# Kernel tuning notes

Measured on AMD Instinct MI355X. Metric: run time of the kernel, lower is better.

Reference implementation:

```python
import jax, jax.numpy as jnp
import numpy as np

DIM = 256
HEAD_DIM = 32
HEADS = DIM // HEAD_DIM
SHAPE = (64, 64)          # (H, W) patch grid
WS = 8                    # window size
SHIFT = 4                 # shift size (ws // 2)
SCALE = HEAD_DIM ** -0.5
WS2 = WS * WS


def _rel_indices(ws):
    # relative position index for every (query, key) pair in a window
    a = np.arange(ws)
    y1, x1, y2, x2 = np.meshgrid(a, a, a, a, indexing='ij')
    idx = (y1 - y2 + ws - 1) * (2 * ws - 1) + (x1 - x2 + ws - 1)
    return idx.reshape(ws * ws, ws * ws)  # (ws2, ws2)


def _shift_mask(shape, ws, shift):
    # region labels per patch, 9 regions from the 3x3 slice grid
    H, W = shape
    region = np.zeros((H, W), dtype=np.int32)
    slices = [slice(0, -ws), slice(-ws, -shift), slice(-shift, None)]
    num = 0
    for i in slices:
        for j in slices:
            region[i, j] = num
            num += 1
    # window-partition the region map -> (n_windows, ws2)
    nH, nW = H // ws, W // ws
    r = region.reshape(nH, ws, nW, ws).transpose(0, 2, 1, 3).reshape(nH * nW, ws * ws)
    # True where query and key come from different regions
    return (r[:, None, :] - r[:, :, None]) != 0  # (nw, ws2, ws2)


REL_IDX = jnp.asarray(_rel_indices(WS))                 # (ws2, ws2) int
MASK = jnp.asarray(_shift_mask(SHAPE, WS, SHIFT))       # (nw, ws2, ws2) bool


def _split_windows(x, ws):
    # (b, H, W, C) -> (b * nH * nW, ws*ws, C)
    b, H, W, C = x.shape
    x = x.reshape(b, H // ws, ws, W // ws, ws, C)
    x = x.transpose(0, 1, 3, 2, 4, 5)
    return x.reshape(-1, ws * ws, C)


def _merge_windows(x, shape, ws):
    # inverse of _split_windows
    H, W = shape
    nH, nW = H // ws, W // ws
    C = x.shape[-1]
    x = x.reshape(-1, nH, nW, ws, ws, C)
    x = x.transpose(0, 1, 3, 2, 4, 5)
    return x.reshape(-1, H, W, C)


def setup_inputs() -> dict:
    key = jax.random.key(0)
    ks = jax.random.split(key, 6)
    s = 0.02
    return {
        'x': jax.random.normal(ks[0], (32, SHAPE[0] * SHAPE[1], DIM), jnp.float32),
        'w_qkv': jax.random.normal(ks[1], (3 * DIM, DIM), jnp.float32) * s,
        'b_qkv': jax.random.normal(ks[2], (3 * DIM,), jnp.float32) * s,
        'w_out': jax.random.normal(ks[3], (DIM, DIM), jnp.float32) * s,
        'b_out': jax.random.normal(ks[4], (DIM,), jnp.float32) * s,
        'pos_enc': jax.random.normal(ks[5], (HEADS, (2 * WS - 1) ** 2), jnp.float32) * s,
    }


def reference(x, w_qkv, b_qkv, w_out, b_out, pos_enc):
    B, N, C = x.shape
    H, W = SHAPE
    nw = (H // WS) * (W // WS)

    xg = x.reshape(B, H, W, C)
    if SHIFT > 0:
        xg = jnp.roll(xg, (-SHIFT, -SHIFT), axis=(1, 2))
    xw = _split_windows(xg, WS)                        # (B*nw, ws2, C)

    qkv = xw @ w_qkv.T + b_qkv                         # (B*nw, ws2, 3C)
    qkv = qkv.reshape(-1, WS2, 3, HEADS, HEAD_DIM)
    q, k, v = (qkv[:, :, i].transpose(0, 2, 1, 3) for i in range(3))  # (Bn, h, ws2, hd)

    attn = jnp.einsum('bhqd,bhkd->bhqk', q, k) * SCALE  # (Bn, h, ws2, ws2)
    bias = pos_enc[:, REL_IDX]                          # (h, ws2, ws2)
    attn = attn + bias[None]

    if SHIFT > 0:
        attn = attn.reshape(B, nw, HEADS, WS2, WS2)
        attn = jnp.where(MASK[None, :, None], -jnp.inf, attn)
        attn = attn.reshape(B * nw, HEADS, WS2, WS2)

    attn = jax.nn.softmax(attn, axis=-1)
    out = jnp.einsum('bhqk,bhkd->bhqd', attn, v)        # (Bn, h, ws2, hd)
    out = out.transpose(0, 2, 1, 3).reshape(-1, WS2, C)
    out = out @ w_out.T + b_out                         # (Bn, ws2, C)

    out = _merge_windows(out, SHAPE, WS)                # (B, H, W, C)
    if SHIFT > 0:
        out = jnp.roll(out, (SHIFT, SHIFT), axis=(1, 2))
    return out.reshape(B, N, C)
```

## Files before the change

kernel.cpp:

```cpp
#include <hip/hip_runtime.h>
#include <stdint.h>


typedef short short8 __attribute__((ext_vector_type(8)));
typedef float f32x4 __attribute__((ext_vector_type(4)));

typedef __attribute__((address_space(1))) uint32_t g_u32;
typedef __attribute__((address_space(3))) uint32_t l_u32;

#define SCALE 0.17677669529663687f

__device__ __forceinline__ uint16_t f2bf(float f) {
  union { float f; uint32_t u; } c; c.f = f;
  uint32_t r = c.u + 0x7FFFu + ((c.u >> 16) & 1u);
  return (uint16_t)(r >> 16);
}

__device__ __forceinline__ void g2lds16(const void* g, void* l) {
  __builtin_amdgcn_global_load_lds((const g_u32*)g, (l_u32*)l, 16, 0, 0);
}

__global__ __launch_bounds__(256) void cvtx_kernel(const float* __restrict__ x,
                                                   uint16_t* __restrict__ xb) {
  int tid = threadIdx.x;
  int token = blockIdx.x * 8 + (tid >> 5);
  int c = (tid & 31) * 8;
  int w = token >> 6, t = token & 63;
  int b = w >> 6, wd = w & 63;
  int h = (wd >> 3) * 8 + (t >> 3);
  int xx = (wd & 7) * 8 + (t & 7);
  int src = b * 4096 + (((h + 4) & 63) << 6) + ((xx + 4) & 63);
  const float* sp = x + (size_t)src * 256 + c;
  f32x4 a = *(const f32x4*)sp;
  f32x4 d = *(const f32x4*)(sp + 4);
  short8 v;
  v[0] = (short)f2bf(a[0]); v[1] = (short)f2bf(a[1]);
  v[2] = (short)f2bf(a[2]); v[3] = (short)f2bf(a[3]);
  v[4] = (short)f2bf(d[0]); v[5] = (short)f2bf(d[1]);
  v[6] = (short)f2bf(d[2]); v[7] = (short)f2bf(d[3]);
  *(short8*)&xb[(size_t)token * 256 + c] = v;
}

__global__ __launch_bounds__(256) void cvt_kernel(const float* __restrict__ in,
                                                  uint16_t* __restrict__ out, int n) {
  int i = (blockIdx.x * 256 + threadIdx.x) * 8;
  if (i >= n) return;
  f32x4 a = *(const f32x4*)(in + i);
  f32x4 b = *(const f32x4*)(in + i + 4);
  short8 v;
  v[0] = (short)f2bf(a[0]); v[1] = (short)f2bf(a[1]);
  v[2] = (short)f2bf(a[2]); v[3] = (short)f2bf(a[3]);
  v[4] = (short)f2bf(b[0]); v[5] = (short)f2bf(b[1]);
  v[6] = (short)f2bf(b[2]); v[7] = (short)f2bf(b[3]);
  *(short8*)(out + i) = v;
}

__global__ __launch_bounds__(256) void bias_kernel(const float* __restrict__ pe,
                                                   float* __restrict__ bm) {
  int bx = blockIdx.x;
  int wd = bx >> 3, head = bx & 7;
  int hw = wd >> 3, ww = wd & 7;
  int tid = threadIdx.x;
  int kk = tid >> 2, a0 = (tid & 3) * 4;
  int jy = kk >> 3, jx = kk & 7;
  int hj = hw * 8 + jy, xj = ww * 8 + jx;
  int rj = (hj >= 60 ? 2 : (hj >= 56 ? 1 : 0)) * 3 + (xj >= 60 ? 2 : (xj >= 56 ? 1 : 0));
  float* dst = bm + (size_t)bx * 4096 + kk * 64 + a0 * 4;
  for (int aa = 0; aa < 4; ++aa) {
    int a = a0 + aa;
    f32x4 v;
#pragma unroll
    for (int ni = 0; ni < 4; ++ni) {
      int i = ni * 16 + a;
      int iy = i >> 3, ix = i & 7;
      int hi = hw * 8 + iy, xi = ww * 8 + ix;
      int ri = (hi >= 60 ? 2 : (hi >= 56 ? 1 : 0)) * 3 + (xi >= 60 ? 2 : (xi >= 56 ? 1 : 0));
      v[ni] = (ri != rj) ? -1e30f : pe[head * 225 + (iy - jy + 7) * 15 + (ix - jx + 7)];
    }
    *(f32x4*)(dst + aa * 4) = v;
  }
}

__global__ __launch_bounds__(256) void qkv_kernel(
    const uint16_t* __restrict__ xb, const uint16_t* __restrict__ wq,
    const float* __restrict__ bqkv,
    uint16_t* __restrict__ qws, uint16_t* __restrict__ kws, uint16_t* __restrict__ vws) {
  __shared__ uint16_t sm[16384];
  uint16_t* As = sm;
  uint16_t* Bs = sm + 4096;
  const int tid = threadIdx.x, lane = tid & 63, wv = tid >> 6;
  const int quad = lane >> 4, l15 = lane & 15;
  const int n0 = blockIdx.x * 128;
  const int m0 = blockIdx.y * 128;

  const int c0 = wv * 2, c1 = c0 + 1;
  const uint16_t* ap0 = xb + (size_t)(m0 + c0 * 16 + (lane >> 2)) * 256 + (lane & 3) * 8;
  const uint16_t* ap1 = xb + (size_t)(m0 + c1 * 16 + (lane >> 2)) * 256 + (lane & 3) * 8;
  const uint16_t* bp0 = wq + (size_t)(n0 + c0 * 16 + (lane >> 2)) * 256 + (lane & 3) * 8;
  const uint16_t* bp1 = wq + (size_t)(n0 + c1 * 16 + (lane >> 2)) * 256 + (lane & 3) * 8;

  const int wm = (wv & 1) * 64, wn = (wv >> 1) * 64;
  f32x4 zero = {0.f, 0.f, 0.f, 0.f};
  f32x4 acc[4][4];
#pragma unroll
  for (int mi = 0; mi < 4; ++mi)
#pragma unroll
    for (int ni = 0; ni < 4; ++ni) acc[mi][ni] = zero;

  for (int ks = 0; ks < 8; ++ks) {
    int k0 = ks * 32;
    g2lds16(ap0 + k0, &As[c0 * 512]);
    g2lds16(ap1 + k0, &As[c1 * 512]);
    g2lds16(bp0 + k0, &Bs[c0 * 512]);
    g2lds16(bp1 + k0, &Bs[c1 * 512]);
    __syncthreads();
    short8 af[4], bf[4];
#pragma unroll
    for (int mi = 0; mi < 4; ++mi)
      af[mi] = *(const short8*)&As[(wm + mi * 16 + l15) * 32 + quad * 8];
#pragma unroll
    for (int ni = 0; ni < 4; ++ni)
      bf[ni] = *(const short8*)&Bs[(wn + ni * 16 + l15) * 32 + quad * 8];
#pragma unroll
    for (int mi = 0; mi < 4; ++mi)
#pragma unroll
      for (int ni = 0; ni < 4; ++ni)
        acc[mi][ni] = __builtin_amdgcn_mfma_f32_16x16x32_bf16(af[mi], bf[ni], acc[mi][ni], 0, 0, 0);
    __syncthreads();
  }

  float bq4[4];
#pragma unroll
  for (int ni = 0; ni < 4; ++ni) bq4[ni] = bqkv[n0 + wn + ni * 16 + l15];
  const int ng0 = n0 + wn;
  const int sct = ng0 >> 8;
  uint16_t* epi = sm + wv * 4096;

  if (sct < 2) {
#pragma unroll
    for (int mi = 0; mi < 4; ++mi)
#pragma unroll
      for (int ni = 0; ni < 4; ++ni)
#pragma unroll
        for (int r = 0; r < 4; ++r) {
          int t = mi * 16 + quad * 4 + r, n = ni * 16 + l15;
          epi[t * 64 + ((((n >> 3) ^ (t & 7)) << 3) | (n & 7))] = f2bf(acc[mi][ni][r] + bq4[ni]);
        }
    uint16_t* dst = (sct == 0) ? qws : kws;
    const int tb = m0 + wm;
#pragma unroll
    for (int cc = 0; cc < 8; ++cc) {
      int chunk = cc * 64 + lane;
      int trow = chunk >> 3, part = chunk & 7;
      short8 v = *(const short8*)&epi[trow * 64 + ((part ^ (trow & 7)) << 3)];
      int tok = tb + trow, w = tok >> 6, t = tok & 63;
      int ng = ng0 + part * 8, hd = (ng >> 5) & 7, d = ng & 31;
      *(short8*)&dst[(size_t)((w * 8 + hd) * 64 + t) * 32 + d] = v;
    }
  } else {
#pragma unroll
    for (int mi = 0; mi < 4; ++mi)
#pragma unroll
      for (int ni = 0; ni < 4; ++ni)
#pragma unroll
        for (int r = 0; r < 4; ++r) {
          int t = mi * 16 + quad * 4 + r, n = ni * 16 + l15;
          epi[n * 64 + ((((t >> 3) ^ (n & 7)) << 3) | (t & 7))] = f2bf(acc[mi][ni][r] + bq4[ni]);
        }
    const int tb = m0 + wm;
#pragma unroll
    for (int cc = 0; cc < 8; ++cc) {
      int chunk = cc * 64 + lane;
      int drow = chunk >> 3, part = chunk & 7;
      short8 v = *(const short8*)&epi[drow * 64 + ((part ^ (drow & 7)) << 3)];
      int ng = ng0 + drow, hd = (ng >> 5) & 7, d = ng & 31;
      int tok = tb + part * 8, w = tok >> 6, t = tok & 63;
      *(short8*)&vws[(size_t)((w * 8 + hd) * 32 + d) * 64 + t] = v;
    }
  }
}

__global__ __launch_bounds__(256) void attn_kernel(
    const uint16_t* __restrict__ qws, const uint16_t* __restrict__ kws,
    const uint16_t* __restrict__ vws, const float* __restrict__ bm,
    uint16_t* __restrict__ ao) {
  __shared__ uint16_t P[4][4096];
  const int tid = threadIdx.x, lane = tid & 63, wv = tid >> 6;
  const int quad = lane >> 4, l15 = lane & 15;
  const int gid = blockIdx.x * 4 + wv;
  const int w = gid >> 3, head = gid & 7;
  const uint16_t* qb = qws + (size_t)(w * 8 + head) * 2048;
  const uint16_t* kb = kws + (size_t)(w * 8 + head) * 2048;
  const uint16_t* vb = vws + (size_t)(w * 8 + head) * 2048;
  const float* bmh = bm + (size_t)((w & 63) * 8 + head) * 4096;
  f32x4 zero = {0.f, 0.f, 0.f, 0.f};

  short8 ak[4], bq[4];
#pragma unroll
  for (int mi = 0; mi < 4; ++mi)
    ak[mi] = *(const short8*)&kb[(mi * 16 + l15) * 32 + quad * 8];
#pragma unroll
  for (int ni = 0; ni < 4; ++ni)
    bq[ni] = *(const short8*)&qb[(ni * 16 + l15) * 32 + quad * 8];

  f32x4 s[4][4];
#pragma unroll
  for (int mi = 0; mi < 4; ++mi)
#pragma unroll
    for (int ni = 0; ni < 4; ++ni)
      s[mi][ni] = __builtin_amdgcn_mfma_f32_16x16x32_bf16(ak[mi], bq[ni], zero, 0, 0, 0);

#pragma unroll
  for (int mi = 0; mi < 4; ++mi)
#pragma unroll
    for (int r = 0; r < 4; ++r) {
      int kk = mi * 16 + quad * 4 + r;
      f32x4 b4 = *(const f32x4*)&bmh[kk * 64 + l15 * 4];
#pragma unroll
      for (int ni = 0; ni < 4; ++ni)
        s[mi][ni][r] = s[mi][ni][r] * SCALE + b4[ni];
    }

#pragma unroll
  for (int ni = 0; ni < 4; ++ni) {
    float mx = s[0][ni][0];
#pragma unroll
    for (int mi = 0; mi < 4; ++mi)
#pragma unroll
      for (int r = 0; r < 4; ++r) mx = fmaxf(mx, s[mi][ni][r]);
    mx = fmaxf(mx, __shfl_xor(mx, 16, 64));
    mx = fmaxf(mx, __shfl_xor(mx, 32, 64));
    float sum = 0.f;
#pragma unroll
    for (int mi = 0; mi < 4; ++mi)
#pragma unroll
      for (int r = 0; r < 4; ++r) {
        float e = __expf(s[mi][ni][r] - mx);
        s[mi][ni][r] = e;
        sum += e;
      }
    sum += __shfl_xor(sum, 16, 64);
    sum += __shfl_xor(sum, 32, 64);
    float inv = 1.f / sum;
#pragma unroll
    for (int mi = 0; mi < 4; ++mi)
#pragma unroll
      for (int r = 0; r < 4; ++r) s[mi][ni][r] *= inv;
  }

  uint16_t* Pw = P[wv];
#pragma unroll
  for (int mi = 0; mi < 4; ++mi)
#pragma unroll
    for (int ni = 0; ni < 4; ++ni)
#pragma unroll
      for (int rp = 0; rp < 2; ++rp) {
        int kk = mi * 16 + quad * 4 + rp * 2;
        int q = ni * 16 + l15;
        uint32_t pk = (uint32_t)f2bf(s[mi][ni][rp * 2]) |
                      ((uint32_t)f2bf(s[mi][ni][rp * 2 + 1]) << 16);
        *(uint32_t*)&Pw[q * 64 + ((((kk >> 3) ^ (q & 7)) << 3) | (kk & 7))] = pk;
      }

  f32x4 o[4][2];
#pragma unroll
  for (int mi = 0; mi < 4; ++mi) { o[mi][0] = zero; o[mi][1] = zero; }
#pragma unroll
  for (int ki = 0; ki < 2; ++ki) {
    short8 vf0 = *(const short8*)&vb[(l15) * 64 + ki * 32 + quad * 8];
    short8 vf1 = *(const short8*)&vb[(16 + l15) * 64 + ki * 32 + quad * 8];
#pragma unroll
    for (int mi = 0; mi < 4; ++mi) {
      int q = mi * 16 + l15;
      short8 pa = *(const short8*)&Pw[q * 64 + (((ki * 4 + quad) ^ (q & 7)) << 3)];
      o[mi][0] = __builtin_amdgcn_mfma_f32_16x16x32_bf16(pa, vf0, o[mi][0], 0, 0, 0);
      o[mi][1] = __builtin_amdgcn_mfma_f32_16x16x32_bf16(pa, vf1, o[mi][1], 0, 0, 0);
    }
  }
#pragma unroll
  for (int mi = 0; mi < 4; ++mi)
#pragma unroll
    for (int ni = 0; ni < 2; ++ni)
#pragma unroll
      for (int r = 0; r < 4; ++r) {
        int t = mi * 16 + quad * 4 + r;
        ao[(size_t)(w * 64 + t) * 256 + head * 32 + ni * 16 + l15] = f2bf(o[mi][ni][r]);
      }
}

__global__ __launch_bounds__(256) void oproj_kernel(
    const uint16_t* __restrict__ aob, const uint16_t* __restrict__ wo,
    const float* __restrict__ bout, float* __restrict__ out) {
  __shared__ uint16_t sm[8192];
  uint16_t* As = sm;
  uint16_t* Bs = sm + 4096;
  const int tid = threadIdx.x, lane = tid & 63, wv = tid >> 6;
  const int quad = lane >> 4, l15 = lane & 15;
  const int n0 = blockIdx.x * 128;
  const int m0 = blockIdx.y * 128;

  const int c0 = wv * 2, c1 = c0 + 1;
  const uint16_t* ap0 = aob + (size_t)(m0 + c0 * 16 + (lane >> 2)) * 256 + (lane & 3) * 8;
  const uint16_t* ap1 = aob + (size_t)(m0 + c1 * 16 + (lane >> 2)) * 256 + (lane & 3) * 8;
  const uint16_t* bp0 = wo + (size_t)(n0 + c0 * 16 + (lane >> 2)) * 256 + (lane & 3) * 8;
  const uint16_t* bp1 = wo + (size_t)(n0 + c1 * 16 + (lane >> 2)) * 256 + (lane & 3) * 8;

  const int wm = (wv & 1) * 64, wn = (wv >> 1) * 64;
  f32x4 zero = {0.f, 0.f, 0.f, 0.f};
  f32x4 acc[4][4];
#pragma unroll
  for (int mi = 0; mi < 4; ++mi)
#pragma unroll
    for (int ni = 0; ni < 4; ++ni) acc[mi][ni] = zero;

  for (int ks = 0; ks < 8; ++ks) {
    int k0 = ks * 32;
    g2lds16(ap0 + k0, &As[c0 * 512]);
    g2lds16(ap1 + k0, &As[c1 * 512]);
    g2lds16(bp0 + k0, &Bs[c0 * 512]);
    g2lds16(bp1 + k0, &Bs[c1 * 512]);
    __syncthreads();
    short8 af[4], bf[4];
#pragma unroll
    for (int mi = 0; mi < 4; ++mi)
      af[mi] = *(const short8*)&As[(wm + mi * 16 + l15) * 32 + quad * 8];
#pragma unroll
    for (int ni = 0; ni < 4; ++ni)
      bf[ni] = *(const short8*)&Bs[(wn + ni * 16 + l15) * 32 + quad * 8];
#pragma unroll
    for (int mi = 0; mi < 4; ++mi)
#pragma unroll
      for (int ni = 0; ni < 4; ++ni)
        acc[mi][ni] = __builtin_amdgcn_mfma_f32_16x16x32_bf16(af[mi], bf[ni], acc[mi][ni], 0, 0, 0);
    __syncthreads();
  }

  float bo4[4];
#pragma unroll
  for (int ni = 0; ni < 4; ++ni) bo4[ni] = bout[n0 + wn + ni * 16 + l15];
#pragma unroll
  for (int mi = 0; mi < 4; ++mi) {
    int mb = m0 + wm + mi * 16 + quad * 4;
    int w = mb >> 6, t0 = mb & 63;
    int b = w >> 6, wd = w & 63;
    int hw2 = wd >> 3, ww2 = wd & 7;
#pragma unroll
    for (int r = 0; r < 4; ++r) {
      int t = t0 + r;
      int h = hw2 * 8 + (t >> 3), xx = ww2 * 8 + (t & 7);
      int row = (((h + 4) & 63) << 6) | ((xx + 4) & 63);
      float* op = out + ((size_t)b * 4096 + row) * 256 + n0 + wn;
#pragma unroll
      for (int ni = 0; ni < 4; ++ni) op[ni * 16 + l15] = acc[mi][ni][r] + bo4[ni];
    }
  }
}

extern "C" void kernel_launch(void* const* d_in, const int* in_sizes, int n_in,
                              void* d_out, int out_size, void* d_ws, size_t ws_size,
                              hipStream_t stream) {
  const float* x = (const float*)d_in[0];
  const float* w_qkv = (const float*)d_in[1];
  const float* b_qkv = (const float*)d_in[2];
  const float* w_out = (const float*)d_in[3];
  const float* b_out = (const float*)d_in[4];
  const float* pos_enc = (const float*)d_in[5];
  float* out = (float*)d_out;

  uint8_t* ws = (uint8_t*)d_ws;
  uint16_t* xb  = (uint16_t*)(ws);
  uint16_t* wqb = (uint16_t*)(ws + 67108864);
  uint16_t* wob = (uint16_t*)(ws + 67502080);
  float*    bmt = (float*)   (ws + 67633152);
  uint16_t* qws = (uint16_t*)(ws + 76021760);
  uint16_t* kws = (uint16_t*)(ws + 143130624);
  uint16_t* vws = (uint16_t*)(ws + 210239488);
  uint16_t* aob = xb;

  cvtx_kernel<<<16384, 256, 0, stream>>>(x, xb);
  cvt_kernel<<<96, 256, 0, stream>>>(w_qkv, wqb, 196608);
  cvt_kernel<<<32, 256, 0, stream>>>(w_out, wob, 65536);
  bias_kernel<<<512, 256, 0, stream>>>(pos_enc, bmt);
  qkv_kernel<<<dim3(6, 1024), 256, 0, stream>>>(xb, wqb, b_qkv, qws, kws, vws);
  attn_kernel<<<4096, 256, 0, stream>>>(qws, kws, vws, bmt, aob);
  oproj_kernel<<<dim3(2, 1024), 256, 0, stream>>>(aob, wob, b_out, out);
}
```

Before: 440.7 us.

## Fuse x conversion into QKV GEMM and output projection into attention

The separate fp32-to-bf16 shifted-window conversion pass is folded into the QKV kernel: each block loads one window of x, converts it to bf16 into swizzled LDS, and loops over all three Q/K/V weight tiles. The output projection is fused into the attention kernel, which now handles one window with all 8 heads, keeps the attention output in LDS and multiplies it by W_out read directly from global memory. The bias/mask table is reduced from 64 windows to 4 window classes in bf16. This removes the xb and attention-output round trips through HBM and two launches, at the cost of larger LDS use per block and lower occupancy.

```diff
diff --git a/kernel.cpp b/kernel.cpp
--- a/kernel.cpp
+++ b/kernel.cpp
@@ -4,6 +4,7 @@
 
 typedef short short8 __attribute__((ext_vector_type(8)));
 typedef float f32x4 __attribute__((ext_vector_type(4)));
+typedef unsigned short ushort4v __attribute__((ext_vector_type(4)));
 
 typedef __attribute__((address_space(1))) uint32_t g_u32;
 typedef __attribute__((address_space(3))) uint32_t l_u32;
@@ -15,30 +16,12 @@
   uint32_t r = c.u + 0x7FFFu + ((c.u >> 16) & 1u);
   return (uint16_t)(r >> 16);
 }
-
+__device__ __forceinline__ float bf2f(uint16_t b) {
+  union { uint32_t u; float f; } c; c.u = ((uint32_t)b) << 16;
+  return c.f;
+}
 __device__ __forceinline__ void g2lds16(const void* g, void* l) {
   __builtin_amdgcn_global_load_lds((const g_u32*)g, (l_u32*)l, 16, 0, 0);
-}
-
-__global__ __launch_bounds__(256) void cvtx_kernel(const float* __restrict__ x,
-                                                   uint16_t* __restrict__ xb) {
-  int tid = threadIdx.x;
-  int token = blockIdx.x * 8 + (tid >> 5);
-  int c = (tid & 31) * 8;
-  int w = token >> 6, t = token & 63;
-  int b = w >> 6, wd = w & 63;
-  int h = (wd >> 3) * 8 + (t >> 3);
-  int xx = (wd & 7) * 8 + (t & 7);
-  int src = b * 4096 + (((h + 4) & 63) << 6) + ((xx + 4) & 63);
-  const float* sp = x + (size_t)src * 256 + c;
-  f32x4 a = *(const f32x4*)sp;
-  f32x4 d = *(const f32x4*)(sp + 4);
-  short8 v;
-  v[0] = (short)f2bf(a[0]); v[1] = (short)f2bf(a[1]);
-  v[2] = (short)f2bf(a[2]); v[3] = (short)f2bf(a[3]);
-  v[4] = (short)f2bf(d[0]); v[5] = (short)f2bf(d[1]);
-  v[6] = (short)f2bf(d[2]); v[7] = (short)f2bf(d[3]);
-  *(short8*)&xb[(size_t)token * 256 + c] = v;
 }
 
 __global__ __launch_bounds__(256) void cvt_kernel(const float* __restrict__ in,
@@ -55,303 +38,306 @@
   *(short8*)(out + i) = v;
 }
 
-__global__ __launch_bounds__(256) void bias_kernel(const float* __restrict__ pe,
-                                                   float* __restrict__ bm) {
+__global__ __launch_bounds__(256) void bmc_kernel(const float* __restrict__ pe,
+                                                  uint16_t* __restrict__ bmc) {
   int bx = blockIdx.x;
-  int wd = bx >> 3, head = bx & 7;
-  int hw = wd >> 3, ww = wd & 7;
+  int cls = bx >> 3, head = bx & 7;
+  int hw7 = cls >> 1, ww7 = cls & 1;
   int tid = threadIdx.x;
   int kk = tid >> 2, a0 = (tid & 3) * 4;
   int jy = kk >> 3, jx = kk & 7;
-  int hj = hw * 8 + jy, xj = ww * 8 + jx;
-  int rj = (hj >= 60 ? 2 : (hj >= 56 ? 1 : 0)) * 3 + (xj >= 60 ? 2 : (xj >= 56 ? 1 : 0));
-  float* dst = bm + (size_t)bx * 4096 + kk * 64 + a0 * 4;
+  int rjy = hw7 ? (1 + (jy >= 4)) : 0;
+  int rjx = ww7 ? (1 + (jx >= 4)) : 0;
+  int rj = rjy * 3 + rjx;
   for (int aa = 0; aa < 4; ++aa) {
     int a = a0 + aa;
-    f32x4 v;
+    ushort4v v;
 #pragma unroll
     for (int ni = 0; ni < 4; ++ni) {
       int i = ni * 16 + a;
       int iy = i >> 3, ix = i & 7;
-      int hi = hw * 8 + iy, xi = ww * 8 + ix;
-      int ri = (hi >= 60 ? 2 : (hi >= 56 ? 1 : 0)) * 3 + (xi >= 60 ? 2 : (xi >= 56 ? 1 : 0));
-      v[ni] = (ri != rj) ? -1e30f : pe[head * 225 + (iy - jy + 7) * 15 + (ix - jx + 7)];
-    }
-    *(f32x4*)(dst + aa * 4) = v;
+      int riy = hw7 ? (1 + (iy >= 4)) : 0;
+      int rix = ww7 ? (1 + (ix >= 4)) : 0;
+      int ri = riy * 3 + rix;
+      float val = (ri != rj) ? -1e30f : pe[head * 225 + (iy - jy + 7) * 15 + (ix - jx + 7)];
+      v[ni] = f2bf(val);
+    }
+    *(ushort4v*)&bmc[(size_t)bx * 4096 + kk * 64 + a * 4] = v;
   }
 }
 
 __global__ __launch_bounds__(256) void qkv_kernel(
-    const uint16_t* __restrict__ xb, const uint16_t* __restrict__ wq,
+    const float* __restrict__ x, const uint16_t* __restrict__ wq,
     const float* __restrict__ bqkv,
     uint16_t* __restrict__ qws, uint16_t* __restrict__ kws, uint16_t* __restrict__ vws) {
-  __shared__ uint16_t sm[16384];
-  uint16_t* As = sm;
-  uint16_t* Bs = sm + 4096;
+  __shared__ uint16_t A[16384];
+  __shared__ uint16_t SH[16384];
   const int tid = threadIdx.x, lane = tid & 63, wv = tid >> 6;
   const int quad = lane >> 4, l15 = lane & 15;
-  const int n0 = blockIdx.x * 128;
-  const int m0 = blockIdx.y * 128;
-
-  const int c0 = wv * 2, c1 = c0 + 1;
-  const uint16_t* ap0 = xb + (size_t)(m0 + c0 * 16 + (lane >> 2)) * 256 + (lane & 3) * 8;
-  const uint16_t* ap1 = xb + (size_t)(m0 + c1 * 16 + (lane >> 2)) * 256 + (lane & 3) * 8;
-  const uint16_t* bp0 = wq + (size_t)(n0 + c0 * 16 + (lane >> 2)) * 256 + (lane & 3) * 8;
-  const uint16_t* bp1 = wq + (size_t)(n0 + c1 * 16 + (lane >> 2)) * 256 + (lane & 3) * 8;
-
-  const int wm = (wv & 1) * 64, wn = (wv >> 1) * 64;
+  const int w = blockIdx.x;
+  const int b = w >> 6, wd = w & 63;
+
+#pragma unroll
+  for (int it = 0; it < 4; ++it) {
+    int row = it * 16 + (tid >> 4);
+    int ch = (tid & 15) * 16;
+    int t = row;
+    int h = (wd >> 3) * 8 + (t >> 3);
+    int xx = (wd & 7) * 8 + (t & 7);
+    int src = b * 4096 + (((h + 4) & 63) << 6) + ((xx + 4) & 63);
+    const float* sp = x + (size_t)src * 256 + ch;
+    f32x4 f0 = *(const f32x4*)sp;
+    f32x4 f1 = *(const f32x4*)(sp + 4);
+    f32x4 f2 = *(const f32x4*)(sp + 8);
+    f32x4 f3 = *(const f32x4*)(sp + 12);
+    short8 v0, v1;
+    v0[0] = (short)f2bf(f0[0]); v0[1] = (short)f2bf(f0[1]);
+    v0[2] = (short)f2bf(f0[2]); v0[3] = (short)f2bf(f0[3]);
+    v0[4] = (short)f2bf(f1[0]); v0[5] = (short)f2bf(f1[1]);
+    v0[6] = (short)f2bf(f1[2]); v0[7] = (short)f2bf(f1[3]);
+    v1[0] = (short)f2bf(f2[0]); v1[1] = (short)f2bf(f2[1]);
+    v1[2] = (short)f2bf(f2[2]); v1[3] = (short)f2bf(f2[3]);
+    v1[4] = (short)f2bf(f3[0]); v1[5] = (short)f2bf(f3[1]);
+    v1[6] = (short)f2bf(f3[2]); v1[7] = (short)f2bf(f3[3]);
+    int g0 = (tid & 15) * 2;
+    *(short8*)&A[row * 256 + ((g0 ^ (row & 7)) << 3)] = v0;
+    *(short8*)&A[row * 256 + (((g0 + 1) ^ (row & 7)) << 3)] = v1;
+  }
+  __syncthreads();
+
   f32x4 zero = {0.f, 0.f, 0.f, 0.f};
-  f32x4 acc[4][4];
-#pragma unroll
-  for (int mi = 0; mi < 4; ++mi)
-#pragma unroll
-    for (int ni = 0; ni < 4; ++ni) acc[mi][ni] = zero;
-
-  for (int ks = 0; ks < 8; ++ks) {
-    int k0 = ks * 32;
-    g2lds16(ap0 + k0, &As[c0 * 512]);
-    g2lds16(ap1 + k0, &As[c1 * 512]);
-    g2lds16(bp0 + k0, &Bs[c0 * 512]);
-    g2lds16(bp1 + k0, &Bs[c1 * 512]);
+  for (int nt = 0; nt < 3; ++nt) {
+    f32x4 acc[4][4];
+#pragma unroll
+    for (int mi = 0; mi < 4; ++mi)
+#pragma unroll
+      for (int ni = 0; ni < 4; ++ni) acc[mi][ni] = zero;
+
+    for (int ks = 0; ks < 8; ++ks) {
+      int k0 = ks * 32;
+#pragma unroll
+      for (int j = 0; j < 4; ++j) {
+        int c = wv * 4 + j;
+        g2lds16(wq + (size_t)(nt * 256 + c * 16 + (lane & 15)) * 256 + k0 + (lane >> 4) * 8,
+                &SH[c * 512]);
+      }
+      __syncthreads();
+      short8 af[4], bf[4];
+#pragma unroll
+      for (int mi = 0; mi < 4; ++mi)
+        af[mi] = *(const short8*)&A[(mi * 16 + l15) * 256 + (((ks * 4 + quad) ^ (l15 & 7)) << 3)];
+#pragma unroll
+      for (int ni = 0; ni < 4; ++ni)
+        bf[ni] = *(const short8*)&SH[(wv * 4 + ni) * 512 + (quad * 16 + l15) * 8];
+#pragma unroll
+      for (int mi = 0; mi < 4; ++mi)
+#pragma unroll
+        for (int ni = 0; ni < 4; ++ni)
+          acc[mi][ni] = __builtin_amdgcn_mfma_f32_16x16x32_bf16(af[mi], bf[ni], acc[mi][ni], 0, 0, 0);
+      __syncthreads();
+    }
+
+    const int ng0 = nt * 256 + wv * 64;
+    float bq4[4];
+#pragma unroll
+    for (int ni = 0; ni < 4; ++ni) bq4[ni] = bqkv[ng0 + ni * 16 + l15];
+    uint16_t* epi = SH + wv * 4096;
+
+    if (nt < 2) {
+#pragma unroll
+      for (int mi = 0; mi < 4; ++mi)
+#pragma unroll
+        for (int ni = 0; ni < 4; ++ni)
+#pragma unroll
+          for (int r = 0; r < 4; ++r) {
+            int t = mi * 16 + quad * 4 + r, n = ni * 16 + l15;
+            epi[t * 64 + ((((n >> 3) ^ (t & 7)) << 3) | (n & 7))] = f2bf(acc[mi][ni][r] + bq4[ni]);
+          }
+      uint16_t* dst = (nt == 0) ? qws : kws;
+#pragma unroll
+      for (int cc = 0; cc < 8; ++cc) {
+        int chunk = cc * 64 + lane;
+        int trow = chunk >> 3, part = chunk & 7;
+        short8 v = *(const short8*)&epi[trow * 64 + ((part ^ (trow & 7)) << 3)];
+        int ng = ng0 + part * 8, hd = (ng >> 5) & 7, d = ng & 31;
+        *(short8*)&dst[(size_t)((w * 8 + hd) * 64 + trow) * 32 + d] = v;
+      }
+    } else {
+#pragma unroll
+      for (int mi = 0; mi < 4; ++mi)
+#pragma unroll
+        for (int ni = 0; ni < 4; ++ni)
+#pragma unroll
+          for (int r = 0; r < 4; ++r) {
+            int t = mi * 16 + quad * 4 + r, n = ni * 16 + l15;
+            epi[n * 64 + ((((t >> 3) ^ (n & 7)) << 3) | (t & 7))] = f2bf(acc[mi][ni][r] + bq4[ni]);
+          }
+#pragma unroll
+      for (int cc = 0; cc < 8; ++cc) {
+        int chunk = cc * 64 + lane;
+        int drow = chunk >> 3, part = chunk & 7;
+        short8 v = *(const short8*)&epi[drow * 64 + ((part ^ (drow & 7)) << 3)];
+        int ng = ng0 + drow, hd = (ng >> 5) & 7, d = ng & 31;
+        *(short8*)&vws[(size_t)((w * 8 + hd) * 32 + d) * 64 + part * 8] = v;
+      }
+    }
     __syncthreads();
-    short8 af[4], bf[4];
-#pragma unroll
-    for (int mi = 0; mi < 4; ++mi)
-      af[mi] = *(const short8*)&As[(wm + mi * 16 + l15) * 32 + quad * 8];
-#pragma unroll
-    for (int ni = 0; ni < 4; ++ni)
-      bf[ni] = *(const short8*)&Bs[(wn + ni * 16 + l15) * 32 + quad * 8];
-#pragma unroll
-    for (int mi = 0; mi < 4; ++mi)
-#pragma unroll
-      for (int ni = 0; ni < 4; ++ni)
-        acc[mi][ni] = __builtin_amdgcn_mfma_f32_16x16x32_bf16(af[mi], bf[ni], acc[mi][ni], 0, 0, 0);
-    __syncthreads();
-  }
-
-  float bq4[4];
-#pragma unroll
-  for (int ni = 0; ni < 4; ++ni) bq4[ni] = bqkv[n0 + wn + ni * 16 + l15];
-  const int ng0 = n0 + wn;
-  const int sct = ng0 >> 8;
-  uint16_t* epi = sm + wv * 4096;
-
-  if (sct < 2) {
-#pragma unroll
-    for (int mi = 0; mi < 4; ++mi)
-#pragma unroll
-      for (int ni = 0; ni < 4; ++ni)
-#pragma unroll
-        for (int r = 0; r < 4; ++r) {
-          int t = mi * 16 + quad * 4 + r, n = ni * 16 + l15;
-          epi[t * 64 + ((((n >> 3) ^ (t & 7)) << 3) | (n & 7))] = f2bf(acc[mi][ni][r] + bq4[ni]);
-        }
-    uint16_t* dst = (sct == 0) ? qws : kws;
-    const int tb = m0 + wm;
-#pragma unroll
-    for (int cc = 0; cc < 8; ++cc) {
-      int chunk = cc * 64 + lane;
-      int trow = chunk >> 3, part = chunk & 7;
-      short8 v = *(const short8*)&epi[trow * 64 + ((part ^ (trow & 7)) << 3)];
-      int tok = tb + trow, w = tok >> 6, t = tok & 63;
-      int ng = ng0 + part * 8, hd = (ng >> 5) & 7, d = ng & 31;
-      *(short8*)&dst[(size_t)((w * 8 + hd) * 64 + t) * 32 + d] = v;
-    }
-  } else {
-#pragma unroll
-    for (int mi = 0; mi < 4; ++mi)
-#pragma unroll
-      for (int ni = 0; ni < 4; ++ni)
-#pragma unroll
-        for (int r = 0; r < 4; ++r) {
-          int t = mi * 16 + quad * 4 + r, n = ni * 16 + l15;
-          epi[n * 64 + ((((t >> 3) ^ (n & 7)) << 3) | (t & 7))] = f2bf(acc[mi][ni][r] + bq4[ni]);
-        }
-    const int tb = m0 + wm;
-#pragma unroll
-    for (int cc = 0; cc < 8; ++cc) {
-      int chunk = cc * 64 + lane;
-      int drow = chunk >> 3, part = chunk & 7;
-      short8 v = *(const short8*)&epi[drow * 64 + ((part ^ (drow & 7)) << 3)];
-      int ng = ng0 + drow, hd = (ng >> 5) & 7, d = ng & 31;
-      int tok = tb + part * 8, w = tok >> 6, t = tok & 63;
-      *(short8*)&vws[(size_t)((w * 8 + hd) * 32 + d) * 64 + t] = v;
-    }
   }
 }
 
 __global__ __launch_bounds__(256) void attn_kernel(
     const uint16_t* __restrict__ qws, const uint16_t* __restrict__ kws,
-    const uint16_t* __restrict__ vws, const float* __restrict__ bm,
-    uint16_t* __restrict__ ao) {
+    const uint16_t* __restrict__ vws, const uint16_t* __restrict__ bmc,
+    const uint16_t* __restrict__ wob, const float* __restrict__ bout,
+    float* __restrict__ out) {
   __shared__ uint16_t P[4][4096];
+  __shared__ uint16_t AO[16384];
   const int tid = threadIdx.x, lane = tid & 63, wv = tid >> 6;
   const int quad = lane >> 4, l15 = lane & 15;
-  const int gid = blockIdx.x * 4 + wv;
-  const int w = gid >> 3, head = gid & 7;
-  const uint16_t* qb = qws + (size_t)(w * 8 + head) * 2048;
-  const uint16_t* kb = kws + (size_t)(w * 8 + head) * 2048;
-  const uint16_t* vb = vws + (size_t)(w * 8 + head) * 2048;
-  const float* bmh = bm + (size_t)((w & 63) * 8 + head) * 4096;
+  const int w = blockIdx.x;
+  const int b = w >> 6, wd = w & 63;
+  const int hw = wd >> 3, ww = wd & 7;
+  const int cls = ((hw == 7) << 1) | (ww == 7);
   f32x4 zero = {0.f, 0.f, 0.f, 0.f};
 
-  short8 ak[4], bq[4];
+  for (int hh = 0; hh < 2; ++hh) {
+    const int head = wv * 2 + hh;
+    const uint16_t* qb = qws + (size_t)(w * 8 + head) * 2048;
+    const uint16_t* kb = kws + (size_t)(w * 8 + head) * 2048;
+    const uint16_t* vb = vws + (size_t)(w * 8 + head) * 2048;
+    const uint16_t* bmh = bmc + (size_t)(cls * 8 + head) * 4096;
+
+    short8 ak[4], bq[4];
+#pragma unroll
+    for (int mi = 0; mi < 4; ++mi)
+      ak[mi] = *(const short8*)&kb[(mi * 16 + l15) * 32 + quad * 8];
+#pragma unroll
+    for (int ni = 0; ni < 4; ++ni)
+      bq[ni] = *(const short8*)&qb[(ni * 16 + l15) * 32 + quad * 8];
+
+    f32x4 s[4][4];
+#pragma unroll
+    for (int mi = 0; mi < 4; ++mi)
+#pragma unroll
+      for (int ni = 0; ni < 4; ++ni)
+        s[mi][ni] = __builtin_amdgcn_mfma_f32_16x16x32_bf16(ak[mi], bq[ni], zero, 0, 0, 0);
+
+#pragma unroll
+    for (int mi = 0; mi < 4; ++mi)
+#pragma unroll
+      for (int r = 0; r < 4; ++r) {
+        int kk = mi * 16 + quad * 4 + r;
+        ushort4v b4 = *(const ushort4v*)&bmh[kk * 64 + l15 * 4];
+#pragma unroll
+        for (int ni = 0; ni < 4; ++ni)
+          s[mi][ni][r] = s[mi][ni][r] * SCALE + bf2f(b4[ni]);
+      }
+
+#pragma unroll
+    for (int ni = 0; ni < 4; ++ni) {
+      float mx = s[0][ni][0];
+#pragma unroll
+      for (int mi = 0; mi < 4; ++mi)
+#pragma unroll
+        for (int r = 0; r < 4; ++r) mx = fmaxf(mx, s[mi][ni][r]);
+      mx = fmaxf(mx, __shfl_xor(mx, 16, 64));
+      mx = fmaxf(mx, __shfl_xor(mx, 32, 64));
+      float sum = 0.f;
+#pragma unroll
+      for (int mi = 0; mi < 4; ++mi)
+#pragma unroll
+        for (int r = 0; r < 4; ++r) {
+          float e = __expf(s[mi][ni][r] - mx);
+          s[mi][ni][r] = e;
+          sum += e;
+        }
+      sum += __shfl_xor(sum, 16, 64);
+      sum += __shfl_xor(sum, 32, 64);
+      float inv = 1.f / sum;
+#pragma unroll
+      for (int mi = 0; mi < 4; ++mi)
+#pragma unroll
+        for (int r = 0; r < 4; ++r) s[mi][ni][r] *= inv;
+    }
+
+    uint16_t* Pw = P[wv];
+#pragma unroll
+    for (int mi = 0; mi < 4; ++mi)
+#pragma unroll
+      for (int ni = 0; ni < 4; ++ni)
+#pragma unroll
+        for (int rp = 0; rp < 2; ++rp) {
+          int kk = mi * 16 + quad * 4 + rp * 2;
+          int q = ni * 16 + l15;
+          uint32_t pk = (uint32_t)f2bf(s[mi][ni][rp * 2]) |
+                        ((uint32_t)f2bf(s[mi][ni][rp * 2 + 1]) << 16);
+          *(uint32_t*)&Pw[q * 64 + ((((kk >> 3) ^ (q & 7)) << 3) | (kk & 7))] = pk;
+        }
+
+    f32x4 o[4][2];
+#pragma unroll
+    for (int mi = 0; mi < 4; ++mi) { o[mi][0] = zero; o[mi][1] = zero; }
+#pragma unroll
+    for (int ki = 0; ki < 2; ++ki) {
+      short8 vf0 = *(const short8*)&vb[(l15) * 64 + ki * 32 + quad * 8];
+      short8 vf1 = *(const short8*)&vb[(16 + l15) * 64 + ki * 32 + quad * 8];
+#pragma unroll
+      for (int mi = 0; mi < 4; ++mi) {
+        int q = mi * 16 + l15;
+        short8 pa = *(const short8*)&Pw[q * 64 + (((ki * 4 + quad) ^ (q & 7)) << 3)];
+        o[mi][0] = __builtin_amdgcn_mfma_f32_16x16x32_bf16(pa, vf0, o[mi][0], 0, 0, 0);
+        o[mi][1] = __builtin_amdgcn_mfma_f32_16x16x32_bf16(pa, vf1, o[mi][1], 0, 0, 0);
+      }
+    }
+#pragma unroll
+    for (int mi = 0; mi < 4; ++mi)
+#pragma unroll
+      for (int ni = 0; ni < 2; ++ni)
+#pragma unroll
+        for (int r = 0; r < 4; ++r) {
+          int t = mi * 16 + quad * 4 + r;
+          int col = head * 32 + ni * 16 + l15;
+          AO[t * 256 + ((((col >> 3) ^ (t & 7)) << 3) | (col & 7))] = f2bf(o[mi][ni][r]);
+        }
+  }
+
+  __syncthreads();
+
+  const int n0 = wv * 64;
+  f32x4 o2[4][4];
 #pragma unroll
   for (int mi = 0; mi < 4; ++mi)
-    ak[mi] = *(const short8*)&kb[(mi * 16 + l15) * 32 + quad * 8];
-#pragma unroll
-  for (int ni = 0; ni < 4; ++ni)
-    bq[ni] = *(const short8*)&qb[(ni * 16 + l15) * 32 + quad * 8];
-
-  f32x4 s[4][4];
-#pragma unroll
-  for (int mi = 0; mi < 4; ++mi)
+#pragma unroll
+    for (int ni = 0; ni < 4; ++ni) o2[mi][ni] = zero;
+  for (int ks = 0; ks < 8; ++ks) {
+    short8 am[4], wb[4];
+#pragma unroll
+    for (int mi = 0; mi < 4; ++mi) {
+      int row = mi * 16 + l15;
+      am[mi] = *(const short8*)&AO[row * 256 + (((ks * 4 + quad) ^ (row & 7)) << 3)];
+    }
 #pragma unroll
     for (int ni = 0; ni < 4; ++ni)
-      s[mi][ni] = __builtin_amdgcn_mfma_f32_16x16x32_bf16(ak[mi], bq[ni], zero, 0, 0, 0);
-
-#pragma unroll
-  for (int mi = 0; mi < 4; ++mi)
+      wb[ni] = *(const short8*)&wob[(size_t)(n0 + ni * 16 + l15) * 256 + ks * 32 + quad * 8];
+#pragma unroll
+    for (int mi = 0; mi < 4; ++mi)
+#pragma unroll
+      for (int ni = 0; ni < 4; ++ni)
+        o2[mi][ni] = __builtin_amdgcn_mfma_f32_16x16x32_bf16(am[mi], wb[ni], o2[mi][ni], 0, 0, 0);
+  }
+  float bo4[4];
+#pragma unroll
+  for (int ni = 0; ni < 4; ++ni) bo4[ni] = bout[n0 + ni * 16 + l15];
+#pragma unroll
+  for (int mi = 0; mi < 4; ++mi) {
 #pragma unroll
     for (int r = 0; r < 4; ++r) {
-      int kk = mi * 16 + quad * 4 + r;
-      f32x4 b4 = *(const f32x4*)&bmh[kk * 64 + l15 * 4];
-#pragma unroll
-      for (int ni = 0; ni < 4; ++ni)
-        s[mi][ni][r] = s[mi][ni][r] * SCALE + b4[ni];
-    }
-
-#pragma unroll
-  for (int ni = 0; ni < 4; ++ni) {
-    float mx = s[0][ni][0];
-#pragma unroll
-    for (int mi = 0; mi < 4; ++mi)
-#pragma unroll
-      for (int r = 0; r < 4; ++r) mx = fmaxf(mx, s[mi][ni][r]);
-    mx = fmaxf(mx, __shfl_xor(mx, 16, 64));
-    mx = fmaxf(mx, __shfl_xor(mx, 32, 64));
-    float sum = 0.f;
-#pragma unroll
-    for (int mi = 0; mi < 4; ++mi)
-#pragma unroll
-      for (int r = 0; r < 4; ++r) {
-        float e = __expf(s[mi][ni][r] - mx);
-        s[mi][ni][r] = e;
-        sum += e;
-      }
-    sum += __shfl_xor(sum, 16, 64);
-    sum += __shfl_xor(sum, 32, 64);
-    float inv = 1.f / sum;
-#pragma unroll
-    for (int mi = 0; mi < 4; ++mi)
-#pragma unroll
-      for (int r = 0; r < 4; ++r) s[mi][ni][r] *= inv;
-  }
-
-  uint16_t* Pw = P[wv];
-#pragma unroll
-  for (int mi = 0; mi < 4; ++mi)
-#pragma unroll
-    for (int ni = 0; ni < 4; ++ni)
-#pragma unroll
-      for (int rp = 0; rp < 2; ++rp) {
-        int kk = mi * 16 + quad * 4 + rp * 2;
-        int q = ni * 16 + l15;
-        uint32_t pk = (uint32_t)f2bf(s[mi][ni][rp * 2]) |
-                      ((uint32_t)f2bf(s[mi][ni][rp * 2 + 1]) << 16);
-        *(uint32_t*)&Pw[q * 64 + ((((kk >> 3) ^ (q & 7)) << 3) | (kk & 7))] = pk;
-      }
-
-  f32x4 o[4][2];
-#pragma unroll
-  for (int mi = 0; mi < 4; ++mi) { o[mi][0] = zero; o[mi][1] = zero; }
-#pragma unroll
-  for (int ki = 0; ki < 2; ++ki) {
-    short8 vf0 = *(const short8*)&vb[(l15) * 64 + ki * 32 + quad * 8];
-    short8 vf1 = *(const short8*)&vb[(16 + l15) * 64 + ki * 32 + quad * 8];
-#pragma unroll
-    for (int mi = 0; mi < 4; ++mi) {
-      int q = mi * 16 + l15;
-      short8 pa = *(const short8*)&Pw[q * 64 + (((ki * 4 + quad) ^ (q & 7)) << 3)];
-      o[mi][0] = __builtin_amdgcn_mfma_f32_16x16x32_bf16(pa, vf0, o[mi][0], 0, 0, 0);
-      o[mi][1] = __builtin_amdgcn_mfma_f32_16x16x32_bf16(pa, vf1, o[mi][1], 0, 0, 0);
-    }
-  }
-#pragma unroll
-  for (int mi = 0; mi < 4; ++mi)
-#pragma unroll
-    for (int ni = 0; ni < 2; ++ni)
-#pragma unroll
-      for (int r = 0; r < 4; ++r) {
-        int t = mi * 16 + quad * 4 + r;
-        ao[(size_t)(w * 64 + t) * 256 + head * 32 + ni * 16 + l15] = f2bf(o[mi][ni][r]);
-      }
-}
-
-__global__ __launch_bounds__(256) void oproj_kernel(
-    const uint16_t* __restrict__ aob, const uint16_t* __restrict__ wo,
-    const float* __restrict__ bout, float* __restrict__ out) {
-  __shared__ uint16_t sm[8192];
-  uint16_t* As = sm;
-  uint16_t* Bs = sm + 4096;
-  const int tid = threadIdx.x, lane = tid & 63, wv = tid >> 6;
-  const int quad = lane >> 4, l15 = lane & 15;
-  const int n0 = blockIdx.x * 128;
-  const int m0 = blockIdx.y * 128;
-
-  const int c0 = wv * 2, c1 = c0 + 1;
-  const uint16_t* ap0 = aob + (size_t)(m0 + c0 * 16 + (lane >> 2)) * 256 + (lane & 3) * 8;
-  const uint16_t* ap1 = aob + (size_t)(m0 + c1 * 16 + (lane >> 2)) * 256 + (lane & 3) * 8;
-  const uint16_t* bp0 = wo + (size_t)(n0 + c0 * 16 + (lane >> 2)) * 256 + (lane & 3) * 8;
-  const uint16_t* bp1 = wo + (size_t)(n0 + c1 * 16 + (lane >> 2)) * 256 + (lane & 3) * 8;
-
-  const int wm = (wv & 1) * 64, wn = (wv >> 1) * 64;
-  f32x4 zero = {0.f, 0.f, 0.f, 0.f};
-  f32x4 acc[4][4];
-#pragma unroll
-  for (int mi = 0; mi < 4; ++mi)
-#pragma unroll
-    for (int ni = 0; ni < 4; ++ni) acc[mi][ni] = zero;
-
-  for (int ks = 0; ks < 8; ++ks) {
-    int k0 = ks * 32;
-    g2lds16(ap0 + k0, &As[c0 * 512]);
-    g2lds16(ap1 + k0, &As[c1 * 512]);
-    g2lds16(bp0 + k0, &Bs[c0 * 512]);
-    g2lds16(bp1 + k0, &Bs[c1 * 512]);
-    __syncthreads();
-    short8 af[4], bf[4];
-#pragma unroll
-    for (int mi = 0; mi < 4; ++mi)
-      af[mi] = *(const short8*)&As[(wm + mi * 16 + l15) * 32 + quad * 8];
-#pragma unroll
-    for (int ni = 0; ni < 4; ++ni)
-      bf[ni] = *(const short8*)&Bs[(wn + ni * 16 + l15) * 32 + quad * 8];
-#pragma unroll
-    for (int mi = 0; mi < 4; ++mi)
-#pragma unroll
-      for (int ni = 0; ni < 4; ++ni)
-        acc[mi][ni] = __builtin_amdgcn_mfma_f32_16x16x32_bf16(af[mi], bf[ni], acc[mi][ni], 0, 0, 0);
-    __syncthreads();
-  }
-
-  float bo4[4];
-#pragma unroll
-  for (int ni = 0; ni < 4; ++ni) bo4[ni] = bout[n0 + wn + ni * 16 + l15];
-#pragma unroll
-  for (int mi = 0; mi < 4; ++mi) {
-    int mb = m0 + wm + mi * 16 + quad * 4;
-    int w = mb >> 6, t0 = mb & 63;
-    int b = w >> 6, wd = w & 63;
-    int hw2 = wd >> 3, ww2 = wd & 7;
-#pragma unroll
-    for (int r = 0; r < 4; ++r) {
-      int t = t0 + r;
-      int h = hw2 * 8 + (t >> 3), xx = ww2 * 8 + (t & 7);
+      int t = mi * 16 + quad * 4 + r;
+      int h = hw * 8 + (t >> 3), xx = ww * 8 + (t & 7);
       int row = (((h + 4) & 63) << 6) | ((xx + 4) & 63);
-      float* op = out + ((size_t)b * 4096 + row) * 256 + n0 + wn;
-#pragma unroll
-      for (int ni = 0; ni < 4; ++ni) op[ni * 16 + l15] = acc[mi][ni][r] + bo4[ni];
+      float* op = out + ((size_t)b * 4096 + row) * 256 + n0;
+#pragma unroll
+      for (int ni = 0; ni < 4; ++ni) op[ni * 16 + l15] = o2[mi][ni][r] + bo4[ni];
     }
   }
 }
@@ -368,20 +354,16 @@
   float* out = (float*)d_out;
 
   uint8_t* ws = (uint8_t*)d_ws;
-  uint16_t* xb  = (uint16_t*)(ws);
-  uint16_t* wqb = (uint16_t*)(ws + 67108864);
-  uint16_t* wob = (uint16_t*)(ws + 67502080);
-  float*    bmt = (float*)   (ws + 67633152);
-  uint16_t* qws = (uint16_t*)(ws + 76021760);
-  uint16_t* kws = (uint16_t*)(ws + 143130624);
-  uint16_t* vws = (uint16_t*)(ws + 210239488);
-  uint16_t* aob = xb;
-
-  cvtx_kernel<<<16384, 256, 0, stream>>>(x, xb);
+  uint16_t* wqb = (uint16_t*)(ws);
+  uint16_t* wob = (uint16_t*)(ws + 393216);
+  uint16_t* bmc = (uint16_t*)(ws + 524288);
+  uint16_t* qws = (uint16_t*)(ws + 786432);
+  uint16_t* kws = (uint16_t*)(ws + 67895296);
+  uint16_t* vws = (uint16_t*)(ws + 135004160);
+
   cvt_kernel<<<96, 256, 0, stream>>>(w_qkv, wqb, 196608);
   cvt_kernel<<<32, 256, 0, stream>>>(w_out, wob, 65536);
-  bias_kernel<<<512, 256, 0, stream>>>(pos_enc, bmt);
-  qkv_kernel<<<dim3(6, 1024), 256, 0, stream>>>(xb, wqb, b_qkv, qws, kws, vws);
-  attn_kernel<<<4096, 256, 0, stream>>>(qws, kws, vws, bmt, aob);
-  oproj_kernel<<<dim3(2, 1024), 256, 0, stream>>>(aob, wob, b_out, out);
-}
+  bmc_kernel<<<32, 256, 0, stream>>>(pos_enc, bmc);
+  qkv_kernel<<<2048, 256, 0, stream>>>(x, wqb, b_qkv, qws, kws, vws);
+  attn_kernel<<<2048, 256, 0, stream>>>(qws, kws, vws, bmc, wob, b_out, out);
+}
```

After: 612.5 us. 1.39x slower.
